# Kernel optimization log

Hardware: AMD Instinct MI355X
Metric: run time of the kernel (lower is better)

## Reference

```python
import jax, jax.numpy as jnp
import numpy as np
from jax import lax

B, C, H, W = 16, 256, 56, 56
MID = 16  # SE: max(C//16, 4)
EPS = 1e-5


def _bn(x, g, b, m, v):
    # inference-mode BatchNorm2d folded to per-channel scale/shift
    s = g * lax.rsqrt(v + EPS)
    return x * s[None, :, None, None] + (b - m * s)[None, :, None, None]


def _dw(x, w, ph, pw):
    # depthwise conv, NCHW, kernel w: [C,1,kh,kw]
    return lax.conv_general_dilated(
        x, w, window_strides=(1, 1), padding=[(ph, ph), (pw, pw)],
        dimension_numbers=('NCHW', 'OIHW', 'NCHW'), feature_group_count=C)


def _pw(x, w):
    # 1x1 conv, w: [O,C,1,1]
    return jnp.einsum('bchw,oc->bohw', x, w[:, :, 0, 0])


def _se(x, w1, b1, w2, b2):
    s = x.mean(axis=(2, 3))                      # [B,C] squeeze
    s = jax.nn.relu(s @ w1.T + b1)               # [B,MID]
    s = jax.nn.sigmoid(s @ w2.T + b2)            # [B,C]
    return x * s[:, :, None, None]


def setup_inputs() -> dict:
    key = jax.random.key(0)
    ks = jax.random.split(key, 32)
    rn = lambda i, shape, sc=0.05: jax.random.normal(ks[i], shape, jnp.float32) * sc
    ru = lambda i, shape: jax.random.uniform(ks[i], shape, jnp.float32)
    return {
        'x': rn(0, (B, C, H, W), 1.0),
        'pw1_w': rn(1, (C, C, 1, 1)),
        'xy3_w': rn(2, (C, 1, 3, 3)), 'xy5_w': rn(3, (C, 1, 5, 5)),
        'bnxy_g': ru(4, (C,)), 'bnxy_b': rn(5, (C,)), 'bnxy_m': rn(6, (C,)), 'bnxy_v': ru(7, (C,)),
        'xz3_w': rn(8, (C, 1, 1, 3)), 'xz5_w': rn(9, (C, 1, 1, 5)),
        'bnxz_g': ru(10, (C,)), 'bnxz_b': rn(11, (C,)), 'bnxz_m': rn(12, (C,)), 'bnxz_v': ru(13, (C,)),
        'yz3_w': rn(14, (C, 1, 3, 1)), 'yz5_w': rn(15, (C, 1, 5, 1)),
        'bnyz_g': ru(16, (C,)), 'bnyz_b': rn(17, (C,)), 'bnyz_m': rn(18, (C,)), 'bnyz_v': ru(19, (C,)),
        'alpha': jnp.full((1, C, 1, 1), 0.5, jnp.float32),
        'beta': jnp.full((1, C, 1, 1), 0.5, jnp.float32),
        'pw2_w': rn(20, (C, C, 1, 1)),
        'bn2_g': ru(21, (C,)), 'bn2_b': rn(22, (C,)), 'bn2_m': rn(23, (C,)), 'bn2_v': ru(24, (C,)),
        'fc1_w': rn(25, (MID, C)), 'fc1_b': rn(26, (MID,)),
        'fc2_w': rn(27, (C, MID)), 'fc2_b': rn(28, (C,)),
    }


def reference(x, pw1_w, xy3_w, xy5_w, bnxy_g, bnxy_b, bnxy_m, bnxy_v,
              xz3_w, xz5_w, bnxz_g, bnxz_b, bnxz_m, bnxz_v,
              yz3_w, yz5_w, bnyz_g, bnyz_b, bnyz_m, bnyz_v,
              alpha, beta, pw2_w, bn2_g, bn2_b, bn2_m, bn2_v,
              fc1_w, fc1_b, fc2_w, fc2_b):
    # Pw1: 1x1 conv, no BN / no act
    out = _pw(x, pw1_w)
    # MS_TOP (stride=1 -> pool is identity)
    # [B] xy branch: DW 3x3 + DW 5x5 -> BN -> ReLU
    f_xy = jax.nn.relu(_bn(_dw(out, xy3_w, 1, 1) + _dw(out, xy5_w, 2, 2),
                           bnxy_g, bnxy_b, bnxy_m, bnxy_v))
    # [A] xz branch: per-row depthwise Conv1d along W == depthwise (1,k) 2D conv
    f_xz = jax.nn.relu(_bn(_dw(out, xz3_w, 0, 1) + _dw(out, xz5_w, 0, 2),
                           bnxz_g, bnxz_b, bnxz_m, bnxz_v))
    # [A] yz branch: per-column depthwise Conv1d along H == depthwise (k,1) 2D conv
    f_yz = jax.nn.relu(_bn(_dw(out, yz3_w, 1, 0) + _dw(out, yz5_w, 2, 0),
                           bnyz_g, bnyz_b, bnyz_m, bnyz_v))
    # [C] learnable-gate fusion
    gate = jax.nn.sigmoid(alpha * f_xz + beta * f_yz)
    top = jax.nn.relu(f_xy * gate)
    # Pw2: 1x1 conv -> BN -> ReLU
    out2 = jax.nn.relu(_bn(_pw(top, pw2_w), bn2_g, bn2_b, bn2_m, bn2_v))
    # SE channel attention
    out2 = _se(out2, fc1_w, fc1_b, fc2_w, fc2_b)
    # DropPath is identity at inference; shortcut is identity (stride=1, in==out)
    return out2 + x
```

## Files before the change

kernel.cpp:

```cpp
#include <hip/hip_runtime.h>
#include <math.h>

typedef __bf16 bf16;
typedef __bf16 bf16x8 __attribute__((ext_vector_type(8)));
typedef __bf16 bf16x4 __attribute__((ext_vector_type(4)));
typedef float f32x4 __attribute__((ext_vector_type(4)));

#define CC 256
#define BB 16
#define HH 56
#define WW 56
#define HWSZ 3136
#define EPS 1e-5f

#define OFF_SCALE 0
#define OFF_SUMS  16384
#define OFF_WBF1  32768
#define OFF_WBF2  163840
#define OFF_WDW   294912
#define OFF_BNC   312832
#define OFF_OUT2  321024

__global__ __launch_bounds__(256) void precast(
    const float* __restrict__ w1, const float* __restrict__ w2,
    const float* __restrict__ xy3, const float* __restrict__ xy5,
    const float* __restrict__ xz3, const float* __restrict__ xz5,
    const float* __restrict__ yz3, const float* __restrict__ yz5,
    const float* __restrict__ gxy, const float* __restrict__ bxy,
    const float* __restrict__ mxy, const float* __restrict__ vxy,
    const float* __restrict__ gxz, const float* __restrict__ bxz,
    const float* __restrict__ mxz, const float* __restrict__ vxz,
    const float* __restrict__ gyz, const float* __restrict__ byz,
    const float* __restrict__ myz, const float* __restrict__ vyz,
    const float* __restrict__ alpha, const float* __restrict__ beta,
    bf16* __restrict__ wbf1, bf16* __restrict__ wbf2,
    bf16* __restrict__ wdw, float* __restrict__ bnc,
    float* __restrict__ sums)
{
    const int blk = blockIdx.x, t = threadIdx.x;
    if (blk < 128) {
        int i = blk * 512 + t * 2;
        wbf1[i] = (bf16)w1[i]; wbf1[i + 1] = (bf16)w1[i + 1];
    } else if (blk < 256) {
        int i = (blk - 128) * 512 + t * 2;
        wbf2[i] = (bf16)w2[i]; wbf2[i + 1] = (bf16)w2[i + 1];
    } else {
        const int c = t;
#pragma unroll
        for (int dh = 0; dh < 5; ++dh)
#pragma unroll
            for (int dw = 0; dw < 5; ++dw) {
                float v = xy5[c * 25 + dh * 5 + dw];
                if (dh >= 1 && dh <= 3 && dw >= 1 && dw <= 3)
                    v += xy3[c * 9 + (dh - 1) * 3 + (dw - 1)];
                wdw[(dh * 5 + dw) * CC + c] = (bf16)v;
            }
#pragma unroll
        for (int d = 0; d < 5; ++d) {
            float v = xz5[c * 5 + d];
            if (d >= 1 && d <= 3) v += xz3[c * 3 + d - 1];
            wdw[(25 + d) * CC + c] = (bf16)v;
            float u = yz5[c * 5 + d];
            if (d >= 1 && d <= 3) u += yz3[c * 3 + d - 1];
            wdw[(30 + d) * CC + c] = (bf16)u;
        }
        float s;
        s = gxy[c] * rsqrtf(vxy[c] + EPS); bnc[0*CC+c] = s; bnc[1*CC+c] = bxy[c] - mxy[c]*s;
        s = gxz[c] * rsqrtf(vxz[c] + EPS); bnc[2*CC+c] = s; bnc[3*CC+c] = bxz[c] - mxz[c]*s;
        s = gyz[c] * rsqrtf(vyz[c] + EPS); bnc[4*CC+c] = s; bnc[5*CC+c] = byz[c] - myz[c]*s;
        bnc[6*CC+c] = alpha[c]; bnc[7*CC+c] = beta[c];
        for (int i = t; i < BB * CC; i += 256) sums[i] = 0.f;
    }
}

__global__ __launch_bounds__(256, 2) void pw_gemm1(
    const float* __restrict__ in, const bf16* __restrict__ wbf,
    bf16* __restrict__ mid)
{
    __shared__ __align__(16) bf16 XT[64][264];
    const int hw0 = blockIdx.x * 64;
    const int b   = blockIdx.y;
    const int t   = threadIdx.x;
    const int lane = t & 63, wv = t >> 6;
    const int q = lane >> 4, n = lane & 15;
    const int co_w = wv * 64;

    bf16x8 aq[4][8];
#pragma unroll
    for (int cf = 0; cf < 4; ++cf) {
        const bf16* wp = wbf + (size_t)(co_w + cf * 16 + n) * CC + q * 8;
#pragma unroll
        for (int kk = 0; kk < 8; ++kk)
            aq[cf][kk] = *(const bf16x8*)(wp + kk * 32);
    }

    {
        const int hwg = (t & 15) * 4;
        const int cig = (t >> 4) * 4;
        const float* base = in + (size_t)b * CC * HWSZ + hw0 + hwg;
#pragma unroll
        for (int pass = 0; pass < 4; ++pass) {
            const int ci0 = pass * 64 + cig;
            f32x4 v[4];
#pragma unroll
            for (int i = 0; i < 4; ++i)
                v[i] = *(const f32x4*)(base + (size_t)(ci0 + i) * HWSZ);
#pragma unroll
            for (int j = 0; j < 4; ++j) {
                bf16x4 r = {(bf16)v[0][j], (bf16)v[1][j], (bf16)v[2][j], (bf16)v[3][j]};
                *(bf16x4*)(&XT[hwg + j][ci0]) = r;
            }
        }
    }
    __syncthreads();

    f32x4 acc[4][4] = {};
#pragma unroll
    for (int kk = 0; kk < 8; ++kk) {
        bf16x8 bq[4];
#pragma unroll
        for (int hf = 0; hf < 4; ++hf)
            bq[hf] = *(const bf16x8*)(&XT[hf * 16 + n][kk * 32 + q * 8]);
#pragma unroll
        for (int cf = 0; cf < 4; ++cf)
#pragma unroll
            for (int hf = 0; hf < 4; ++hf)
                acc[cf][hf] = __builtin_amdgcn_mfma_f32_16x16x32_bf16(
                    aq[cf][kk], bq[hf], acc[cf][hf], 0, 0, 0);
    }

    bf16* ob = mid + ((size_t)b * HWSZ + hw0) * CC;
#pragma unroll
    for (int cf = 0; cf < 4; ++cf) {
        const int co4 = co_w + cf * 16 + q * 4;
#pragma unroll
        for (int hf = 0; hf < 4; ++hf) {
            bf16x4 r = {(bf16)acc[cf][hf][0], (bf16)acc[cf][hf][1],
                        (bf16)acc[cf][hf][2], (bf16)acc[cf][hf][3]};
            *(bf16x4*)(ob + (size_t)(hf * 16 + n) * CC + co4) = r;
        }
    }
}

__global__ __launch_bounds__(256) void dwfuse(
    const bf16* __restrict__ mid, const bf16* __restrict__ wdw,
    const float* __restrict__ bnc, bf16* __restrict__ top)
{
    __shared__ __align__(16) float lwf[35 * 256];
    const int t = threadIdx.x;
#pragma unroll
    for (int k = 0; k < 35; ++k)
        lwf[k * 256 + t] = (float)wdw[k * 256 + t];
    __syncthreads();

    const int lane = t & 63;
    const int wb = blockIdx.x * 8 + (t >> 6) * 2;
    const int h0 = blockIdx.y * 2;
    const size_t plane = (size_t)blockIdx.z * HWSZ;
    const int c0 = lane * 4;

    f32x4 axy[2][2] = {}, axz[2][2] = {}, ayz[2][2] = {};

#pragma unroll
    for (int dhh = 0; dhh < 6; ++dhh) {
        const int hh = h0 - 2 + dhh;
        if ((unsigned)hh >= (unsigned)HH) continue;
        const bf16* rowp = mid + (plane + (size_t)hh * WW) * CC + c0;

        f32x4 fv[6];
#pragma unroll
        for (int wc = 0; wc < 6; ++wc) {
            const int ww = wb - 2 + wc;
            f32x4 f = {0.f, 0.f, 0.f, 0.f};
            if ((unsigned)ww < (unsigned)WW) {
                bf16x4 v = *(const bf16x4*)(rowp + (size_t)ww * CC);
                f[0] = (float)v[0]; f[1] = (float)v[1];
                f[2] = (float)v[2]; f[3] = (float)v[3];
            }
            fv[wc] = f;
        }

#pragma unroll
        for (int ph = 0; ph < 2; ++ph) {
            const int dh = dhh - ph;
            if (dh < 0 || dh > 4) continue;
#pragma unroll
            for (int dw = 0; dw < 5; ++dw) {
                const f32x4 wt = *(const f32x4*)(&lwf[(dh * 5 + dw) * CC + c0]);
                axy[ph][0] += wt * fv[dw];
                axy[ph][1] += wt * fv[dw + 1];
            }
            if (dh == 2) {
#pragma unroll
                for (int dw = 0; dw < 5; ++dw) {
                    const f32x4 wt = *(const f32x4*)(&lwf[(25 + dw) * CC + c0]);
                    axz[ph][0] += wt * fv[dw];
                    axz[ph][1] += wt * fv[dw + 1];
                }
            }
            {
                const f32x4 wt = *(const f32x4*)(&lwf[(30 + dh) * CC + c0]);
                ayz[ph][0] += wt * fv[2];
                ayz[ph][1] += wt * fv[3];
            }
        }
    }

    const f32x4 sxy = *(const f32x4*)(bnc + 0 * CC + c0);
    const f32x4 hxy = *(const f32x4*)(bnc + 1 * CC + c0);
    const f32x4 sxz = *(const f32x4*)(bnc + 2 * CC + c0);
    const f32x4 hxz = *(const f32x4*)(bnc + 3 * CC + c0);
    const f32x4 syz = *(const f32x4*)(bnc + 4 * CC + c0);
    const f32x4 hyz = *(const f32x4*)(bnc + 5 * CC + c0);
    const f32x4 al  = *(const f32x4*)(bnc + 6 * CC + c0);
    const f32x4 be  = *(const f32x4*)(bnc + 7 * CC + c0);

#pragma unroll
    for (int ph = 0; ph < 2; ++ph)
#pragma unroll
        for (int pw = 0; pw < 2; ++pw) {
            const f32x4 txy = axy[ph][pw] * sxy + hxy;
            const f32x4 txz = axz[ph][pw] * sxz + hxz;
            const f32x4 tyz = ayz[ph][pw] * syz + hyz;
            bf16x4 r;
#pragma unroll
            for (int j = 0; j < 4; ++j) {
                const float fxy = fmaxf(txy[j], 0.f);
                const float fxz = fmaxf(txz[j], 0.f);
                const float fyz = fmaxf(tyz[j], 0.f);
                const float z   = al[j] * fxz + be[j] * fyz;
                const float g   = 1.f / (1.f + __expf(-z));
                r[j] = (bf16)(fxy * g);
            }
            *(bf16x4*)(top + (plane + (size_t)(h0 + ph) * WW + (wb + pw)) * CC + c0) = r;
        }
}

__global__ __launch_bounds__(256, 2) void pw_gemm2(
    const bf16* __restrict__ top, const bf16* __restrict__ wbf,
    const float* __restrict__ g2, const float* __restrict__ b2,
    const float* __restrict__ m2, const float* __restrict__ v2,
    bf16* __restrict__ out2, float* __restrict__ sums)
{
    __shared__ __align__(16) bf16 XT[64][264];
    const int hw0 = blockIdx.x * 64;
    const int b   = blockIdx.y;
    const int t   = threadIdx.x;
    const int lane = t & 63, wv = t >> 6;
    const int q = lane >> 4, n = lane & 15;
    const int co_w = wv * 64;

    bf16x8 aq[4][8];
#pragma unroll
    for (int cf = 0; cf < 4; ++cf) {
        const bf16* wp = wbf + (size_t)(co_w + cf * 16 + n) * CC + q * 8;
#pragma unroll
        for (int kk = 0; kk < 8; ++kk)
            aq[cf][kk] = *(const bf16x8*)(wp + kk * 32);
    }

    {
        const int hw_r = t >> 2;
        const int k0   = (t & 3) * 64;
        const bf16* src = top + ((size_t)b * HWSZ + hw0 + hw_r) * CC + k0;
#pragma unroll
        for (int j = 0; j < 8; ++j)
            *(bf16x8*)(&XT[hw_r][k0 + j * 8]) = *(const bf16x8*)(src + j * 8);
    }
    __syncthreads();

    f32x4 acc[4][4] = {};
#pragma unroll
    for (int kk = 0; kk < 8; ++kk) {
        bf16x8 bq[4];
#pragma unroll
        for (int hf = 0; hf < 4; ++hf)
            bq[hf] = *(const bf16x8*)(&XT[hf * 16 + n][kk * 32 + q * 8]);
#pragma unroll
        for (int cf = 0; cf < 4; ++cf)
#pragma unroll
            for (int hf = 0; hf < 4; ++hf)
                acc[cf][hf] = __builtin_amdgcn_mfma_f32_16x16x32_bf16(
                    aq[cf][kk], bq[hf], acc[cf][hf], 0, 0, 0);
    }

    bf16* ob = out2 + ((size_t)b * HWSZ + hw0) * CC;
#pragma unroll
    for (int cf = 0; cf < 4; ++cf) {
        const int co4 = co_w + cf * 16 + q * 4;
        f32x4 g = *(const f32x4*)(g2 + co4);
        f32x4 bb = *(const f32x4*)(b2 + co4);
        f32x4 mm = *(const f32x4*)(m2 + co4);
        f32x4 vv = *(const f32x4*)(v2 + co4);
        f32x4 sc, sh;
#pragma unroll
        for (int r = 0; r < 4; ++r) {
            sc[r] = g[r] * rsqrtf(vv[r] + EPS);
            sh[r] = bb[r] - mm[r] * sc[r];
        }
        f32x4 rs = {};
#pragma unroll
        for (int hf = 0; hf < 4; ++hf) {
            bf16x4 r4;
#pragma unroll
            for (int r = 0; r < 4; ++r) {
                float v = fmaxf(acc[cf][hf][r] * sc[r] + sh[r], 0.f);
                rs[r] += v;
                r4[r] = (bf16)v;
            }
            *(bf16x4*)(ob + (size_t)(hf * 16 + n) * CC + co4) = r4;
        }
#pragma unroll
        for (int msk = 1; msk < 16; msk <<= 1)
#pragma unroll
            for (int r = 0; r < 4; ++r) rs[r] += __shfl_xor(rs[r], msk);
        if (n == 0) {
#pragma unroll
            for (int r = 0; r < 4; ++r)
                atomicAdd(&sums[b * CC + co4 + r], rs[r]);
        }
    }
}

__global__ __launch_bounds__(256) void se_fc(
    const float* __restrict__ sums,
    const float* __restrict__ w1, const float* __restrict__ b1,
    const float* __restrict__ w2, const float* __restrict__ b2,
    float* __restrict__ scale)
{
    __shared__ float mean[256];
    __shared__ float hid[16];
    const int b = blockIdx.x, tid = threadIdx.x;
    mean[tid] = sums[b * CC + tid] * (1.f / (float)HWSZ);
    __syncthreads();
    if (tid < 16) {
        float h = b1[tid];
        for (int cd = 0; cd < 256; ++cd) h += w1[tid * 256 + cd] * mean[cd];
        hid[tid] = fmaxf(h, 0.f);
    }
    __syncthreads();
    float v = b2[tid];
#pragma unroll
    for (int md = 0; md < 16; ++md) v += w2[tid * 16 + md] * hid[md];
    scale[b * CC + tid] = 1.f / (1.f + expf(-v));
}

__global__ __launch_bounds__(256) void se_apply(
    const bf16* __restrict__ out2, const float* __restrict__ x,
    const float* __restrict__ scale, float* __restrict__ out)
{
    __shared__ float TT[64 * 68];
    const int hw0 = blockIdx.x * 64;
    const int c0  = blockIdx.y * 64;
    const int b   = blockIdx.z;
    const int t   = threadIdx.x;

    {
        const int hw_r = t >> 2;
        const int coff = (t & 3) * 16;
        const bf16* p = out2 + ((size_t)b * HWSZ + hw0 + hw_r) * CC + c0 + coff;
        bf16x8 u0 = *(const bf16x8*)(p);
        bf16x8 u1 = *(const bf16x8*)(p + 8);
        const float* sp = scale + b * CC + c0 + coff;
        f32x4 s0 = *(const f32x4*)(sp), s1 = *(const f32x4*)(sp + 4);
        f32x4 s2 = *(const f32x4*)(sp + 8), s3 = *(const f32x4*)(sp + 12);
#pragma unroll
        for (int j = 0; j < 4; ++j) {
            TT[(coff + j)      * 68 + hw_r] = (float)u0[j]     * s0[j];
            TT[(coff + 4 + j)  * 68 + hw_r] = (float)u0[4 + j] * s1[j];
            TT[(coff + 8 + j)  * 68 + hw_r] = (float)u1[j]     * s2[j];
            TT[(coff + 12 + j) * 68 + hw_r] = (float)u1[4 + j] * s3[j];
        }
    }
    __syncthreads();
    {
        const int c_r   = t >> 2;
        const int hwoff = (t & 3) * 16;
        const size_t go = ((size_t)b * CC + c0 + c_r) * HWSZ + hw0 + hwoff;
#pragma unroll
        for (int v = 0; v < 4; ++v) {
            f32x4 tv = *(const f32x4*)(&TT[c_r * 68 + hwoff + v * 4]);
            f32x4 xv = *(const f32x4*)(x + go + v * 4);
#pragma unroll
            for (int j = 0; j < 4; ++j) tv[j] += xv[j];
            *(f32x4*)(out + go + v * 4) = tv;
        }
    }
}

extern "C" void kernel_launch(void* const* d_in, const int* in_sizes, int n_in,
                              void* d_out, int out_size, void* d_ws, size_t ws_size,
                              hipStream_t stream)
{
    const float* x      = (const float*)d_in[0];
    const float* pw1_w  = (const float*)d_in[1];
    const float* xy3_w  = (const float*)d_in[2];
    const float* xy5_w  = (const float*)d_in[3];
    const float* bnxy_g = (const float*)d_in[4];
    const float* bnxy_b = (const float*)d_in[5];
    const float* bnxy_m = (const float*)d_in[6];
    const float* bnxy_v = (const float*)d_in[7];
    const float* xz3_w  = (const float*)d_in[8];
    const float* xz5_w  = (const float*)d_in[9];
    const float* bnxz_g = (const float*)d_in[10];
    const float* bnxz_b = (const float*)d_in[11];
    const float* bnxz_m = (const float*)d_in[12];
    const float* bnxz_v = (const float*)d_in[13];
    const float* yz3_w  = (const float*)d_in[14];
    const float* yz5_w  = (const float*)d_in[15];
    const float* bnyz_g = (const float*)d_in[16];
    const float* bnyz_b = (const float*)d_in[17];
    const float* bnyz_m = (const float*)d_in[18];
    const float* bnyz_v = (const float*)d_in[19];
    const float* alpha  = (const float*)d_in[20];
    const float* beta   = (const float*)d_in[21];
    const float* pw2_w  = (const float*)d_in[22];
    const float* bn2_g  = (const float*)d_in[23];
    const float* bn2_b  = (const float*)d_in[24];
    const float* bn2_m  = (const float*)d_in[25];
    const float* bn2_v  = (const float*)d_in[26];
    const float* fc1_w  = (const float*)d_in[27];
    const float* fc1_b  = (const float*)d_in[28];
    const float* fc2_w  = (const float*)d_in[29];
    const float* fc2_b  = (const float*)d_in[30];

    const size_t NEL = (size_t)BB * CC * HWSZ;
    char* ws = (char*)d_ws;
    float* scale = (float*)(ws + OFF_SCALE);
    float* sums  = (float*)(ws + OFF_SUMS);
    bf16*  wbf1  = (bf16*) (ws + OFF_WBF1);
    bf16*  wbf2  = (bf16*) (ws + OFF_WBF2);
    bf16*  wdw   = (bf16*) (ws + OFF_WDW);
    float* bnc   = (float*)(ws + OFF_BNC);
    bf16*  out2  = (bf16*) (ws + OFF_OUT2);
    bf16*  mid   = (bf16*)d_out;
    bf16*  top   = (bf16*)d_out + NEL;

    precast<<<257, 256, 0, stream>>>(pw1_w, pw2_w,
        xy3_w, xy5_w, xz3_w, xz5_w, yz3_w, yz5_w,
        bnxy_g, bnxy_b, bnxy_m, bnxy_v,
        bnxz_g, bnxz_b, bnxz_m, bnxz_v,
        bnyz_g, bnyz_b, bnyz_m, bnyz_v,
        alpha, beta, wbf1, wbf2, wdw, bnc, sums);

    pw_gemm1<<<dim3(49, 16), 256, 0, stream>>>(x, wbf1, mid);
    dwfuse<<<dim3(7, 28, 16), 256, 0, stream>>>(mid, wdw, bnc, top);
    pw_gemm2<<<dim3(49, 16), 256, 0, stream>>>(top, wbf2, bn2_g, bn2_b,
                                               bn2_m, bn2_v, out2, sums);
    se_fc<<<BB, 256, 0, stream>>>(sums, fc1_w, fc1_b, fc2_w, fc2_b, scale);
    se_apply<<<dim3(49, 4, 16), 256, 0, stream>>>(out2, x, scale, (float*)d_out);
}
```

Baseline: 294.3 us.

## Halve GEMM weight register footprint for 3 blocks/CU; store DW weights as bf16

Both pointwise GEMM kernels now keep only half of the K-dimension weight fragments in registers at a time. The second half is reloaded from global memory after the first four K steps, and launch bounds rise to 3 blocks per CU to raise occupancy. The depthwise kernel stores its filter weights in LDS as bf16 instead of float, which halves LDS use, and converts bf16 to fp32 with bit shifts. The trade-off is a mid-loop global weight reload that may stall the MFMA stream, plus extra ALU work per weight read in the depthwise kernel.

```diff
diff --git a/kernel.cpp b/kernel.cpp
--- a/kernel.cpp
+++ b/kernel.cpp
@@ -20,6 +20,16 @@
 #define OFF_WDW   294912
 #define OFF_BNC   312832
 #define OFF_OUT2  321024
+
+__device__ __forceinline__ f32x4 cvt4(bf16x4 v) {
+    union { bf16x4 b; unsigned int u[2]; } q; q.b = v;
+    f32x4 r;
+    r[0] = __uint_as_float(q.u[0] << 16);
+    r[1] = __uint_as_float(q.u[0] & 0xffff0000u);
+    r[2] = __uint_as_float(q.u[1] << 16);
+    r[3] = __uint_as_float(q.u[1] & 0xffff0000u);
+    return r;
+}
 
 __global__ __launch_bounds__(256) void precast(
     const float* __restrict__ w1, const float* __restrict__ w2,
@@ -73,7 +83,7 @@
     }
 }
 
-__global__ __launch_bounds__(256, 2) void pw_gemm1(
+__global__ __launch_bounds__(256, 3) void pw_gemm1(
     const float* __restrict__ in, const bf16* __restrict__ wbf,
     bf16* __restrict__ mid)
 {
@@ -85,13 +95,14 @@
     const int q = lane >> 4, n = lane & 15;
     const int co_w = wv * 64;
 
-    bf16x8 aq[4][8];
+    bf16x8 aq[4][4];
+    const bf16* wp[4];
 #pragma unroll
     for (int cf = 0; cf < 4; ++cf) {
-        const bf16* wp = wbf + (size_t)(co_w + cf * 16 + n) * CC + q * 8;
-#pragma unroll
-        for (int kk = 0; kk < 8; ++kk)
-            aq[cf][kk] = *(const bf16x8*)(wp + kk * 32);
+        wp[cf] = wbf + (size_t)(co_w + cf * 16 + n) * CC + q * 8;
+#pragma unroll
+        for (int kx = 0; kx < 4; ++kx)
+            aq[cf][kx] = *(const bf16x8*)(wp[cf] + kx * 32);
     }
 
     {
@@ -116,17 +127,28 @@
 
     f32x4 acc[4][4] = {};
 #pragma unroll
-    for (int kk = 0; kk < 8; ++kk) {
-        bf16x8 bq[4];
-#pragma unroll
-        for (int hf = 0; hf < 4; ++hf)
-            bq[hf] = *(const bf16x8*)(&XT[hf * 16 + n][kk * 32 + q * 8]);
-#pragma unroll
-        for (int cf = 0; cf < 4; ++cf)
+    for (int half = 0; half < 2; ++half) {
+#pragma unroll
+        for (int kx = 0; kx < 4; ++kx) {
+            const int kk = half * 4 + kx;
+            bf16x8 bq[4];
 #pragma unroll
             for (int hf = 0; hf < 4; ++hf)
-                acc[cf][hf] = __builtin_amdgcn_mfma_f32_16x16x32_bf16(
-                    aq[cf][kk], bq[hf], acc[cf][hf], 0, 0, 0);
+                bq[hf] = *(const bf16x8*)(&XT[hf * 16 + n][kk * 32 + q * 8]);
+#pragma unroll
+            for (int cf = 0; cf < 4; ++cf)
+#pragma unroll
+                for (int hf = 0; hf < 4; ++hf)
+                    acc[cf][hf] = __builtin_amdgcn_mfma_f32_16x16x32_bf16(
+                        aq[cf][kx], bq[hf], acc[cf][hf], 0, 0, 0);
+        }
+        if (half == 0) {
+#pragma unroll
+            for (int cf = 0; cf < 4; ++cf)
+#pragma unroll
+                for (int kx = 0; kx < 4; ++kx)
+                    aq[cf][kx] = *(const bf16x8*)(wp[cf] + 128 + kx * 32);
+        }
     }
 
     bf16* ob = mid + ((size_t)b * HWSZ + hw0) * CC;
@@ -146,11 +168,13 @@
     const bf16* __restrict__ mid, const bf16* __restrict__ wdw,
     const float* __restrict__ bnc, bf16* __restrict__ top)
 {
-    __shared__ __align__(16) float lwf[35 * 256];
+    __shared__ __align__(16) bf16 lw[35 * 256];
     const int t = threadIdx.x;
 #pragma unroll
-    for (int k = 0; k < 35; ++k)
-        lwf[k * 256 + t] = (float)wdw[k * 256 + t];
+    for (int i = 0; i < 4; ++i)
+        *(bf16x8*)(&lw[(i * 256 + t) * 8]) = *(const bf16x8*)(wdw + (i * 256 + t) * 8);
+    if (t < 96)
+        *(bf16x8*)(&lw[(1024 + t) * 8]) = *(const bf16x8*)(wdw + (1024 + t) * 8);
     __syncthreads();
 
     const int lane = t & 63;
@@ -172,11 +196,8 @@
         for (int wc = 0; wc < 6; ++wc) {
             const int ww = wb - 2 + wc;
             f32x4 f = {0.f, 0.f, 0.f, 0.f};
-            if ((unsigned)ww < (unsigned)WW) {
-                bf16x4 v = *(const bf16x4*)(rowp + (size_t)ww * CC);
-                f[0] = (float)v[0]; f[1] = (float)v[1];
-                f[2] = (float)v[2]; f[3] = (float)v[3];
-            }
+            if ((unsigned)ww < (unsigned)WW)
+                f = cvt4(*(const bf16x4*)(rowp + (size_t)ww * CC));
             fv[wc] = f;
         }
 
@@ -186,20 +207,20 @@
             if (dh < 0 || dh > 4) continue;
 #pragma unroll
             for (int dw = 0; dw < 5; ++dw) {
-                const f32x4 wt = *(const f32x4*)(&lwf[(dh * 5 + dw) * CC + c0]);
+                const f32x4 wt = cvt4(*(const bf16x4*)(&lw[(dh * 5 + dw) * CC + c0]));
                 axy[ph][0] += wt * fv[dw];
                 axy[ph][1] += wt * fv[dw + 1];
             }
             if (dh == 2) {
 #pragma unroll
                 for (int dw = 0; dw < 5; ++dw) {
-                    const f32x4 wt = *(const f32x4*)(&lwf[(25 + dw) * CC + c0]);
+                    const f32x4 wt = cvt4(*(const bf16x4*)(&lw[(25 + dw) * CC + c0]));
                     axz[ph][0] += wt * fv[dw];
                     axz[ph][1] += wt * fv[dw + 1];
                 }
             }
             {
-                const f32x4 wt = *(const f32x4*)(&lwf[(30 + dh) * CC + c0]);
+                const f32x4 wt = cvt4(*(const bf16x4*)(&lw[(30 + dh) * CC + c0]));
                 ayz[ph][0] += wt * fv[2];
                 ayz[ph][1] += wt * fv[3];
             }
@@ -236,7 +257,7 @@
         }
 }
 
-__global__ __launch_bounds__(256, 2) void pw_gemm2(
+__global__ __launch_bounds__(256, 3) void pw_gemm2(
     const bf16* __restrict__ top, const bf16* __restrict__ wbf,
     const float* __restrict__ g2, const float* __restrict__ b2,
     const float* __restrict__ m2, const float* __restrict__ v2,
@@ -250,13 +271,14 @@
     const int q = lane >> 4, n = lane & 15;
     const int co_w = wv * 64;
 
-    bf16x8 aq[4][8];
+    bf16x8 aq[4][4];
+    const bf16* wp[4];
 #pragma unroll
     for (int cf = 0; cf < 4; ++cf) {
-        const bf16* wp = wbf + (size_t)(co_w + cf * 16 + n) * CC + q * 8;
-#pragma unroll
-        for (int kk = 0; kk < 8; ++kk)
-            aq[cf][kk] = *(const bf16x8*)(wp + kk * 32);
+        wp[cf] = wbf + (size_t)(co_w + cf * 16 + n) * CC + q * 8;
+#pragma unroll
+        for (int kx = 0; kx < 4; ++kx)
+            aq[cf][kx] = *(const bf16x8*)(wp[cf] + kx * 32);
     }
 
     {
@@ -271,17 +293,28 @@
 
     f32x4 acc[4][4] = {};
 #pragma unroll
-    for (int kk = 0; kk < 8; ++kk) {
-        bf16x8 bq[4];
-#pragma unroll
-        for (int hf = 0; hf < 4; ++hf)
-            bq[hf] = *(const bf16x8*)(&XT[hf * 16 + n][kk * 32 + q * 8]);
-#pragma unroll
-        for (int cf = 0; cf < 4; ++cf)
+    for (int half = 0; half < 2; ++half) {
+#pragma unroll
+        for (int kx = 0; kx < 4; ++kx) {
+            const int kk = half * 4 + kx;
+            bf16x8 bq[4];
 #pragma unroll
             for (int hf = 0; hf < 4; ++hf)
-                acc[cf][hf] = __builtin_amdgcn_mfma_f32_16x16x32_bf16(
-                    aq[cf][kk], bq[hf], acc[cf][hf], 0, 0, 0);
+                bq[hf] = *(const bf16x8*)(&XT[hf * 16 + n][kk * 32 + q * 8]);
+#pragma unroll
+            for (int cf = 0; cf < 4; ++cf)
+#pragma unroll
+                for (int hf = 0; hf < 4; ++hf)
+                    acc[cf][hf] = __builtin_amdgcn_mfma_f32_16x16x32_bf16(
+                        aq[cf][kx], bq[hf], acc[cf][hf], 0, 0, 0);
+        }
+        if (half == 0) {
+#pragma unroll
+            for (int cf = 0; cf < 4; ++cf)
+#pragma unroll
+                for (int kx = 0; kx < 4; ++kx)
+                    aq[cf][kx] = *(const bf16x8*)(wp[cf] + 128 + kx * 32);
+        }
     }
 
     bf16* ob = out2 + ((size_t)b * HWSZ + hw0) * CC;
```

Result: no change. 291.9 us (-0.8%).
